# Performance work log

Measured on AMD Instinct MI355X. Metric: run time of the kernel, lower is better.

The kernel has to match this reference:

```python
import jax, jax.numpy as jnp
import numpy as np

EPS = 1e-5

def _bn(x, g, b):
    # BatchNorm1d in training mode: biased batch variance, eps=1e-5
    mu = jnp.mean(x, axis=0)
    var = jnp.var(x, axis=0)
    return g * (x - mu) * jax.lax.rsqrt(var + EPS) + b

def _prelu(x, a):
    return jnp.where(x >= 0, x, a * x)

def setup_inputs() -> dict:
    key = jax.random.key(0)
    ks = jax.random.split(key, 32)
    B, MF, E = 4096, 128, 64
    f32 = jnp.float32

    def lin_w(k, o, i):
        bound = 1.0 / np.sqrt(i)
        return jax.random.uniform(k, (o, i), f32, -bound, bound)

    def lin_b(k, o, i):
        bound = 1.0 / np.sqrt(i)
        return jax.random.uniform(k, (o,), f32, -bound, bound)

    def exp_w(k, e, o, i):
        bound = 1.0 / np.sqrt(i)
        return jax.random.uniform(k, (e, o, i), f32, -bound, bound)

    def exp_b(k, e, o, i):
        bound = 1.0 / np.sqrt(i)
        return jax.random.uniform(k, (e, o), f32, -bound, bound)

    quarter = jnp.full((1,), 0.25, f32)  # PReLU default init
    return {
        'm0': jax.random.normal(ks[0], (B, MF), f32),
        'x0': jax.random.normal(ks[1], (B, 64), f32),
        'mW1': lin_w(ks[2], 256, 128), 'mb1': lin_b(ks[3], 256, 128),
        'mg1': jnp.ones((256,), f32), 'mbe1': jnp.zeros((256,), f32), 'ma1': quarter,
        'mW2': lin_w(ks[4], 128, 256), 'mb2': lin_b(ks[5], 128, 256),
        'mg2': jnp.ones((128,), f32), 'mbe2': jnp.zeros((128,), f32), 'ma2': quarter,
        'mW3': lin_w(ks[6], 64, 128), 'mb3': lin_b(ks[7], 64, 128),
        'mg3': jnp.ones((64,), f32), 'mbe3': jnp.zeros((64,), f32), 'ma3': quarter,
        'Wenc0': exp_w(ks[8], E, 256, 64), 'benc0': exp_b(ks[9], E, 256, 64),
        'Wenc1': exp_w(ks[10], E, 256, 256), 'benc1': exp_b(ks[11], E, 256, 256),
        'Wdec0': exp_w(ks[12], E, 256, 256), 'bdec0': exp_b(ks[13], E, 256, 256),
        'Wdec1': exp_w(ks[14], E, 64, 256), 'bdec1': exp_b(ks[15], E, 64, 256),
        'bng': jnp.ones((256,), f32), 'bnb': jnp.zeros((256,), f32), 'a': quarter,
    }

def reference(m0, x0, mW1, mb1, mg1, mbe1, ma1, mW2, mb2, mg2, mbe2, ma2,
              mW3, mb3, mg3, mbe3, ma3, Wenc0, benc0, Wenc1, benc1,
              Wdec0, bdec0, Wdec1, bdec1, bng, bnb, a):
    # m_encoder (MNet): Linear+BN+PReLU x3 -> per-sample expert weights [B, 64]
    h = _prelu(_bn(m0 @ mW1.T + mb1, mg1, mbe1), ma1)
    h = _prelu(_bn(h @ mW2.T + mb2, mg2, mbe2), ma2)
    w = _prelu(_bn(h @ mW3.T + mb3, mg3, mbe3), ma3)  # [B, E]

    w_sum = jnp.sum(w)           # scalar sum over all B*E, as in torch code
    wn = w / w_sum               # [B, E]

    def experts(z, W, b):
        # all-experts dense combine: sum_e wn[b,e] * (z @ W_e^T + b_e)
        h = jnp.einsum('bi,eoi->beo', z, W) + b  # [B, E, O]
        return jnp.einsum('beo,be->bo', h, wn)

    # encoder: depth=2, BN+PReLU after each layer (shared bn(256) and PReLU)
    z = _prelu(_bn(experts(x0, Wenc0, benc0), bng, bnb), a)
    z = _prelu(_bn(experts(z, Wenc1, benc1), bng, bnb), a)
    # decoder: BN+PReLU on all but last layer
    y = _prelu(_bn(experts(z, Wdec0, bdec0), bng, bnb), a)
    y = experts(y, Wdec1, bdec1)  # [B, 64]
    return y
```

## Files before the change

kernel.cpp:

```cpp
#include <hip/hip_runtime.h>
#include <stdint.h>

#define BATCH 4096
#define NEXP 64

typedef __bf16 bf16x8 __attribute__((ext_vector_type(8)));
typedef float f32x4 __attribute__((ext_vector_type(4)));
typedef float f32x8 __attribute__((ext_vector_type(8)));
typedef unsigned int u32x4 __attribute__((ext_vector_type(4)));
typedef unsigned short u16x4 __attribute__((ext_vector_type(4)));
typedef unsigned short u16x8 __attribute__((ext_vector_type(8)));

__device__ __forceinline__ unsigned short f2bf(float f) {
  unsigned u = __builtin_bit_cast(unsigned, f);
  u += 0x7fffu + ((u >> 16) & 1u);
  return (unsigned short)(u >> 16);
}
__device__ __forceinline__ float bf2f(unsigned short h) {
  unsigned u = ((unsigned)h) << 16;
  return __builtin_bit_cast(float, u);
}

__device__ __forceinline__ void async_copy16(const void* g, void* l) {
  __builtin_amdgcn_global_load_lds(
      (const __attribute__((address_space(1))) void*)(uintptr_t)g,
      (__attribute__((address_space(3))) void*)(uintptr_t)l, 16, 0, 0);
}

enum { AM_PLAIN = 0, AM_BN = 1 };

template <int BM_, int BN_, int WR, int WC, int AMODE>
__global__ __launch_bounds__(256, 4) void gemm_k(
    const float* __restrict__ Af32, const float* __restrict__ scv,
    const float* __restrict__ shv, const float* __restrict__ alphaPtr,
    const unsigned short* __restrict__ PB, int K, int nsubsTot,
    float* __restrict__ Cp, const float* __restrict__ biasv, int N,
    int ktilesTot) {
  constexpr int MS = BM_ / 16;
  constexpr int NS = BN_ / 16;
  constexpr int WTM = BM_ / WR, WTN = BN_ / WC;
  constexpr int TM = WTM / 16, TN = WTN / 16;
  constexpr int PCH = MS / 2;

  __shared__ __align__(16) unsigned short As[2 * MS * 512];
  __shared__ __align__(16) unsigned short Bs[2 * NS * 512];

  const int tid = threadIdx.x;
  const int lane = tid & 63;
  const int wid = tid >> 6;
  const int wrow = wid / WC, wcol = wid % WC;

  const int m0 = blockIdx.x * BM_;
  const int ntile = blockIdx.y;
  const int n0 = ntile * BN_;

  float alpha = 0.f;
  if constexpr (AMODE == AM_BN) alpha = alphaPtr[0];

  f32x4 acc[TM][TN] = {};

  for (int kt = 0; kt < ktilesTot; ++kt) {
    const int k0 = kt * 64;

    for (int f = wid; f < 2 * NS; f += 4) {
      const int fkt = f / NS, fns = f % NS;
      const long fragIdx = (long)(k0 / 32 + fkt) * nsubsTot + (ntile * NS + fns);
      async_copy16(PB + fragIdx * 512 + lane * 8, &Bs[f * 512 + lane * 8]);
    }

#pragma unroll
    for (int p = 0; p < PCH; ++p) {
      const int id = p * 256 + tid;
      const int fA = id >> 6;
      const int q = id & 63;
      const int ksh = fA / MS, msub = fA % MS;
      const int kq = q >> 4, mrow = q & 15;
      const int m = msub * 16 + mrow;
      const int kg = k0 + ksh * 32 + kq * 8;
      const long mg = m0 + m;
      f32x8 vf;
      if constexpr (AMODE == AM_PLAIN) {
        const f32x4* src = (const f32x4*)(Af32 + mg * K + kg);
        f32x4 a0 = src[0], a1 = src[1];
#pragma unroll
        for (int j = 0; j < 4; ++j) { vf[j] = a0[j]; vf[4 + j] = a1[j]; }
      } else {
        const f32x4* src = (const f32x4*)(Af32 + mg * K + kg);
        f32x4 a0 = src[0], a1 = src[1];
        f32x4 s0 = *(const f32x4*)(scv + kg), s1 = *(const f32x4*)(scv + kg + 4);
        f32x4 h0 = *(const f32x4*)(shv + kg), h1 = *(const f32x4*)(shv + kg + 4);
#pragma unroll
        for (int j = 0; j < 4; ++j) {
          float v = fmaf(a0[j], s0[j], h0[j]);
          vf[j] = v >= 0.f ? v : alpha * v;
          float v2 = fmaf(a1[j], s1[j], h1[j]);
          vf[4 + j] = v2 >= 0.f ? v2 : alpha * v2;
        }
      }
      bf16x8 ob = __builtin_convertvector(vf, bf16x8);
      *(u16x8*)&As[id * 8] = __builtin_bit_cast(u16x8, ob);
    }
    __syncthreads();

#pragma unroll
    for (int ks = 0; ks < 2; ++ks) {
      bf16x8 af[TM], bfr[TN];
#pragma unroll
      for (int i = 0; i < TM; ++i) {
        const int msub = wrow * TM + i;
        af[i] = __builtin_bit_cast(
            bf16x8, *(const u32x4*)&As[(ks * MS + msub) * 512 + lane * 8]);
      }
#pragma unroll
      for (int j = 0; j < TN; ++j) {
        const int nsub = wcol * TN + j;
        bfr[j] = __builtin_bit_cast(
            bf16x8, *(const u32x4*)&Bs[(ks * NS + nsub) * 512 + lane * 8]);
      }
#pragma unroll
      for (int i = 0; i < TM; ++i)
#pragma unroll
        for (int j = 0; j < TN; ++j)
          acc[i][j] = __builtin_amdgcn_mfma_f32_16x16x32_bf16(af[i], bfr[j],
                                                              acc[i][j], 0, 0, 0);
    }
    __syncthreads();
  }

  const int q = lane >> 4, nn = lane & 15;
#pragma unroll
  for (int i = 0; i < TM; ++i) {
    const int rowb = m0 + wrow * WTM + i * 16 + q * 4;
#pragma unroll
    for (int j = 0; j < TN; ++j) {
      const int col = n0 + wcol * WTN + j * 16 + nn;
      const float bv = biasv ? biasv[col] : 0.f;
#pragma unroll
      for (int r = 0; r < 4; ++r)
        Cp[(long)(rowb + r) * N + col] = acc[i][j][r] + bv;
    }
  }
}

template <int BN_, int KE_, int EPB, int NTILE>
__global__ __launch_bounds__(256, 2) void egemm_k(
    const unsigned short* __restrict__ zpk, const float* __restrict__ wnT,
    const float* __restrict__ bias, const unsigned short* __restrict__ PB,
    float* __restrict__ Cbase, long partStride, int N, int nsubsTot) {
  constexpr int KT2 = KE_ / 32;
  constexpr int NS = BN_ / 16;
  constexpr int TN = NS / 4;
  constexpr int TM = 4;
  constexpr int NC = NTILE * (NEXP / EPB);
  constexpr int T = EPB * KT2;
  constexpr int U = ((KT2 & 3) == 0) ? 1 : (4 / KT2);

  const int tid = threadIdx.x, lane = tid & 63, wid = tid >> 6;
  const int bx = blockIdx.x;
  const int combo = bx % NC;
  const int mb = bx / NC;
  const int ntile = combo % NTILE;
  const int slice = combo / NTILE;
  const int e0 = slice * EPB;
  const int n0 = ntile * BN_;
  float* __restrict__ Cp = Cbase + (long)slice * partStride;
  const int nn = lane & 15, q = lane >> 4;

  const unsigned short* Aw = zpk + (long)mb * (KT2 * 4 * 512);
  u32x4 areg[TM][KT2];
#pragma unroll
  for (int i = 0; i < TM; ++i)
#pragma unroll
    for (int kt = 0; kt < KT2; ++kt)
      areg[i][kt] = *(const u32x4*)(Aw + (kt * 4 + i) * 512 + lane * 8);

  const long kstr = (long)nsubsTot * 512;
  const unsigned short* Bt = PB + (long)e0 * KT2 * kstr +
                             ((long)ntile * NS + wid * TN) * 512 + lane * 8;

  u32x4 ring[4][TN];
#pragma unroll
  for (int t = 0; t < 4; ++t)
#pragma unroll
    for (int j = 0; j < TN; ++j)
      ring[t][j] = *(const u32x4*)(Bt + (long)t * kstr + j * 512);

  f32x4 mainAcc[TM][TN] = {};

  for (int eb = 0; eb < EPB; eb += U) {
#pragma unroll
    for (int u = 0; u < U; ++u) {
      const int ei = eb + u;
      const int e = e0 + ei;
      f32x4 tmp[TM][TN];
#pragma unroll
      for (int j = 0; j < TN; ++j) {
        const float bv = bias[(long)e * N + n0 + wid * (TN * 16) + j * 16 + nn];
        f32x4 t4 = {bv, bv, bv, bv};
#pragma unroll
        for (int i = 0; i < TM; ++i) tmp[i][j] = t4;
      }
#pragma unroll
      for (int kt = 0; kt < KT2; ++kt) {
        const int slot = (u * KT2 + kt) & 3;
#pragma unroll
        for (int i = 0; i < TM; ++i) {
          bf16x8 af = __builtin_bit_cast(bf16x8, areg[i][kt]);
#pragma unroll
          for (int j = 0; j < TN; ++j)
            tmp[i][j] = __builtin_amdgcn_mfma_f32_16x16x32_bf16(
                af, __builtin_bit_cast(bf16x8, ring[slot][j]), tmp[i][j], 0, 0,
                0);
        }
        {
          const int t = ei * KT2 + kt;
          const int tl = (t + 4 < T) ? (t + 4) : (T - 1);
#pragma unroll
          for (int j = 0; j < TN; ++j)
            ring[slot][j] = *(const u32x4*)(Bt + (long)tl * kstr + j * 512);
        }
      }
#pragma unroll
      for (int i = 0; i < TM; ++i) {
        const int rowb = mb * 64 + i * 16 + q * 4;
        f32x4 wn4 = *(const f32x4*)(wnT + (long)e * BATCH + rowb);
#pragma unroll
        for (int j = 0; j < TN; ++j) mainAcc[i][j] += wn4 * tmp[i][j];
      }
    }
  }

#pragma unroll
  for (int i = 0; i < TM; ++i) {
    const int rowb = mb * 64 + i * 16 + q * 4;
#pragma unroll
    for (int j = 0; j < TN; ++j) {
      const int col = n0 + wid * (TN * 16) + j * 16 + nn;
#pragma unroll
      for (int r = 0; r < 4; ++r)
        Cp[(long)(rowb + r) * N + col] = mainAcc[i][j][r];
    }
  }
}

__global__ void hbuild_k(float* __restrict__ P, long partStride, int nparts,
                         int total4) {
  const int idx = blockIdx.x * 256 + threadIdx.x;
  if (idx >= total4) return;
  f32x4 s = *(const f32x4*)(P + (long)idx * 4);
  for (int p = 1; p < nparts; ++p)
    s += *(const f32x4*)(P + p * partStride + (long)idx * 4);
  *(f32x4*)(P + (long)idx * 4) = s;
}

__global__ void stats_k(const float* __restrict__ H, int C,
                        const float* __restrict__ g, const float* __restrict__ b,
                        float* __restrict__ scv, float* __restrict__ shv) {
  const int c0 = blockIdx.x * 4;
  f32x4 s = {0.f, 0.f, 0.f, 0.f}, s2 = {0.f, 0.f, 0.f, 0.f};
  for (int r = threadIdx.x; r < BATCH; r += 256) {
    f32x4 x = *(const f32x4*)(H + (long)r * C + c0);
    s += x;
    s2 += x * x;
  }
  __shared__ f32x4 sb[256], qb[256];
  sb[threadIdx.x] = s;
  qb[threadIdx.x] = s2;
  __syncthreads();
  for (int st = 128; st > 0; st >>= 1) {
    if (threadIdx.x < st) {
      sb[threadIdx.x] += sb[threadIdx.x + st];
      qb[threadIdx.x] += qb[threadIdx.x + st];
    }
    __syncthreads();
  }
  if (threadIdx.x < 4) {
    const int c = c0 + threadIdx.x;
    float mu = sb[0][threadIdx.x] * (1.f / BATCH);
    float var = qb[0][threadIdx.x] * (1.f / BATCH) - mu * mu;
    float isig = 1.f / sqrtf(var + 1e-5f);
    float sc_ = g[c] * isig;
    scv[c] = sc_;
    shv[c] = b[c] - mu * sc_;
  }
}

__global__ void zbuild_pk(const float* __restrict__ H,
                          const float* __restrict__ scv,
                          const float* __restrict__ shv,
                          const float* __restrict__ alphaPtr,
                          unsigned short* __restrict__ zpk) {
  const int c = blockIdx.x * 256 + threadIdx.x;
  const float alpha = alphaPtr[0];
  const int mb = c >> 11, r = c & 2047;
  const int kt = r >> 8, q2 = r & 255;
  const int msub = q2 >> 6, ln = q2 & 63;
  const int row = mb * 64 + msub * 16 + (ln & 15);
  const int col = kt * 32 + (ln >> 4) * 8;
  const float* src = H + (long)row * 256 + col;
  f32x4 a0 = *(const f32x4*)src, a1 = *(const f32x4*)(src + 4);
  f32x4 s0 = *(const f32x4*)(scv + col), s1 = *(const f32x4*)(scv + col + 4);
  f32x4 h0 = *(const f32x4*)(shv + col), h1 = *(const f32x4*)(shv + col + 4);
  u16x8 o;
#pragma unroll
  for (int j = 0; j < 4; ++j) {
    float v = fmaf(a0[j], s0[j], h0[j]);
    v = v >= 0.f ? v : alpha * v;
    o[j] = f2bf(v);
    float v2 = fmaf(a1[j], s1[j], h1[j]);
    v2 = v2 >= 0.f ? v2 : alpha * v2;
    o[4 + j] = f2bf(v2);
  }
  *(u16x8*)(zpk + (long)c * 8) = o;
}

__global__ void cast_pk(const float* __restrict__ x,
                        unsigned short* __restrict__ zpk) {
  const int c = blockIdx.x * 256 + threadIdx.x;
  const int mb = c >> 9, r = c & 511;
  const int kt = r >> 8, q2 = r & 255;
  const int msub = q2 >> 6, ln = q2 & 63;
  const int row = mb * 64 + msub * 16 + (ln & 15);
  const int col = kt * 32 + (ln >> 4) * 8;
  const float* src = x + (long)row * 64 + col;
  f32x4 a0 = *(const f32x4*)src, a1 = *(const f32x4*)(src + 4);
  u16x8 o;
#pragma unroll
  for (int j = 0; j < 4; ++j) {
    o[j] = f2bf(a0[j]);
    o[4 + j] = f2bf(a1[j]);
  }
  *(u16x8*)(zpk + (long)c * 8) = o;
}

__global__ void wbuild_k(const float* __restrict__ G, const float* __restrict__ scv,
                         const float* __restrict__ shv,
                         const float* __restrict__ alphaPtr,
                         float* __restrict__ w, float* __restrict__ wsum) {
  const int idx = blockIdx.x * 256 + threadIdx.x;
  const float alpha = alphaPtr[0];
  const int c0 = (idx * 4) & 63;
  f32x4 x = *(const f32x4*)(G + (long)idx * 4);
  f32x4 sv = *(const f32x4*)(scv + c0);
  f32x4 hv = *(const f32x4*)(shv + c0);
  f32x4 o;
  float part = 0.f;
#pragma unroll
  for (int j = 0; j < 4; ++j) {
    float v = fmaf(x[j], sv[j], hv[j]);
    v = v >= 0.f ? v : alpha * v;
    o[j] = v;
    part += v;
  }
  *(f32x4*)(w + (long)idx * 4) = o;
  __shared__ float sb[256];
  sb[threadIdx.x] = part;
  __syncthreads();
  for (int st = 128; st > 0; st >>= 1) {
    if (threadIdx.x < st) sb[threadIdx.x] += sb[threadIdx.x + st];
    __syncthreads();
  }
  if (threadIdx.x == 0) atomicAdd(wsum, sb[0]);
}

__global__ void inv_k(const float* __restrict__ wsum, float* __restrict__ invp) {
  if (threadIdx.x == 0 && blockIdx.x == 0) invp[0] = 1.0f / wsum[0];
}

__global__ void wntbuild_k(const float* __restrict__ w,
                           const float* __restrict__ invp,
                           float* __restrict__ wnT) {
  const int idx = blockIdx.x * 256 + threadIdx.x;
  const int e = idx >> 12, b = idx & 4095;
  wnT[idx] = w[(long)b * NEXP + e] * invp[0];
}

__global__ void prepack_k(const float* __restrict__ W, const float* __restrict__ bias,
                          unsigned short* __restrict__ PB, int O, int shI, int EI,
                          long totalChunks) {
  const long t = (long)blockIdx.x * 256 + threadIdx.x;
  if (t >= totalChunks) return;
  const int lane = (int)(t & 63);
  const long frag = t >> 6;
  const int nsubs = O / 16;
  const int nsub = (int)(frag % nsubs);
  const long ktile = frag / nsubs;
  const int n = nsub * 16 + (lane & 15);
  const int k = (int)(ktile * 32 + (lane >> 4) * 8);
  u16x8 o;
  if (k < EI) {
    const int e = k >> shI;
    const int i0 = k & ((1 << shI) - 1);
    const float* src = W + ((long)e * O + n) * (1 << shI) + i0;
    f32x4 a0 = *(const f32x4*)src;
    f32x4 a1 = *(const f32x4*)(src + 4);
#pragma unroll
    for (int j = 0; j < 4; ++j) {
      o[j] = f2bf(a0[j]);
      o[4 + j] = f2bf(a1[j]);
    }
  } else {
#pragma unroll
    for (int j = 0; j < 8; ++j) {
      const int ee = k + j - EI;
      o[j] = f2bf(bias[(long)ee * O + n]);
    }
  }
  *(u16x8*)(PB + t * 8) = o;
}

__global__ void reduceN_k(const float* __restrict__ P, long partStride, int nparts,
                          float* __restrict__ out, int total4) {
  const int idx = blockIdx.x * 256 + threadIdx.x;
  if (idx >= total4) return;
  f32x4 s = {0.f, 0.f, 0.f, 0.f};
  for (int p = 0; p < nparts; ++p) s += *(const f32x4*)(P + p * partStride + (long)idx * 4);
  *(f32x4*)(out + (long)idx * 4) = s;
}

extern "C" void kernel_launch(void* const* d_in, const int* in_sizes, int n_in,
                              void* d_out, int out_size, void* d_ws, size_t ws_size,
                              hipStream_t stream) {
  const float* m0 = (const float*)d_in[0];
  const float* x0 = (const float*)d_in[1];
  const float* mW1 = (const float*)d_in[2];
  const float* mb1 = (const float*)d_in[3];
  const float* mg1 = (const float*)d_in[4];
  const float* mbe1 = (const float*)d_in[5];
  const float* ma1 = (const float*)d_in[6];
  const float* mW2 = (const float*)d_in[7];
  const float* mb2 = (const float*)d_in[8];
  const float* mg2 = (const float*)d_in[9];
  const float* mbe2 = (const float*)d_in[10];
  const float* ma2 = (const float*)d_in[11];
  const float* mW3 = (const float*)d_in[12];
  const float* mb3 = (const float*)d_in[13];
  const float* mg3 = (const float*)d_in[14];
  const float* mbe3 = (const float*)d_in[15];
  const float* ma3 = (const float*)d_in[16];
  const float* Wenc0 = (const float*)d_in[17];
  const float* benc0 = (const float*)d_in[18];
  const float* Wenc1 = (const float*)d_in[19];
  const float* benc1 = (const float*)d_in[20];
  const float* Wdec0 = (const float*)d_in[21];
  const float* bdec0 = (const float*)d_in[22];
  const float* Wdec1 = (const float*)d_in[23];
  const float* bdec1 = (const float*)d_in[24];
  const float* bng = (const float*)d_in[25];
  const float* bnb = (const float*)d_in[26];
  const float* aexp = (const float*)d_in[27];

  const int SPL = 8, SPLD = 16;

  char* base = (char*)d_ws;
  size_t off = 0;
  auto alloc = [&](size_t bytes) {
    void* p = base + off;
    off = (off + bytes + 255) & ~(size_t)255;
    return p;
  };
  unsigned short* PB = (unsigned short*)alloc(16448L * 256 * 2);
  float* Pb = (float*)alloc((size_t)SPL * BATCH * 256 * 4);
  float* P0 = Pb;
  float* P1 = Pb + (long)BATCH * 256;
  unsigned short* zApk = (unsigned short*)alloc(BATCH * 256 * 2);
  unsigned short* zBpk = (unsigned short*)alloc(BATCH * 256 * 2);
  unsigned short* x0pk = (unsigned short*)alloc(BATCH * 64 * 2);
  float* wbuf = (float*)alloc(BATCH * 64 * 4);
  float* wnT = (float*)alloc((size_t)NEXP * BATCH * 4);
  float* scv = (float*)alloc(256 * 4);
  float* shv = (float*)alloc(256 * 4);
  float* wsum = (float*)alloc(256);
  float* invp = (float*)alloc(256);

  const dim3 blk(256);
  const long PS = BATCH * 256;

  prepack_k<<<16, blk, 0, stream>>>(mW1, nullptr, PB, 256, 7, 128, 4096);
  gemm_k<64, 128, 2, 2, AM_PLAIN><<<dim3(64, 2, 1), blk, 0, stream>>>(
      m0, nullptr, nullptr, nullptr, PB, 128, 16, P0, mb1, 256, 2);
  stats_k<<<64, blk, 0, stream>>>(P0, 256, mg1, mbe1, scv, shv);

  prepack_k<<<16, blk, 0, stream>>>(mW2, nullptr, PB, 128, 8, 256, 4096);
  gemm_k<64, 128, 2, 2, AM_BN><<<dim3(64, 1, 1), blk, 0, stream>>>(
      P0, scv, shv, ma1, PB, 256, 8, P1, mb2, 128, 4);
  stats_k<<<32, blk, 0, stream>>>(P1, 128, mg2, mbe2, scv, shv);

  prepack_k<<<4, blk, 0, stream>>>(mW3, nullptr, PB, 64, 7, 128, 1024);
  gemm_k<64, 64, 2, 2, AM_BN><<<dim3(64, 1, 1), blk, 0, stream>>>(
      P1, scv, shv, ma2, PB, 128, 4, P0, mb3, 64, 2);
  stats_k<<<16, blk, 0, stream>>>(P0, 64, mg3, mbe3, scv, shv);

  hipMemsetAsync(wsum, 0, 4, stream);
  wbuild_k<<<256, blk, 0, stream>>>(P0, scv, shv, ma3, wbuf, wsum);
  inv_k<<<1, 64, 0, stream>>>(wsum, invp);
  wntbuild_k<<<1024, blk, 0, stream>>>(wbuf, invp, wnT);
  cast_pk<<<128, blk, 0, stream>>>(x0, x0pk);

  prepack_k<<<512, blk, 0, stream>>>(Wenc0, nullptr, PB, 256, 6, 4096, 131072);
  egemm_k<128, 64, 8, 2><<<dim3(1024), blk, 0, stream>>>(
      x0pk, wnT, benc0, PB, Pb, PS, 256, 16);
  hbuild_k<<<1024, blk, 0, stream>>>(Pb, PS, SPL, 262144);
  stats_k<<<64, blk, 0, stream>>>(Pb, 256, bng, bnb, scv, shv);
  zbuild_pk<<<512, blk, 0, stream>>>(Pb, scv, shv, aexp, zApk);

  prepack_k<<<2048, blk, 0, stream>>>(Wenc1, nullptr, PB, 256, 8, 16384, 524288);
  egemm_k<128, 256, 8, 2><<<dim3(1024), blk, 0, stream>>>(
      zApk, wnT, benc1, PB, Pb, PS, 256, 16);
  hbuild_k<<<1024, blk, 0, stream>>>(Pb, PS, SPL, 262144);
  stats_k<<<64, blk, 0, stream>>>(Pb, 256, bng, bnb, scv, shv);
  zbuild_pk<<<512, blk, 0, stream>>>(Pb, scv, shv, aexp, zBpk);

  prepack_k<<<2048, blk, 0, stream>>>(Wdec0, nullptr, PB, 256, 8, 16384, 524288);
  egemm_k<128, 256, 8, 2><<<dim3(1024), blk, 0, stream>>>(
      zBpk, wnT, bdec0, PB, Pb, PS, 256, 16);
  hbuild_k<<<1024, blk, 0, stream>>>(Pb, PS, SPL, 262144);
  stats_k<<<64, blk, 0, stream>>>(Pb, 256, bng, bnb, scv, shv);
  zbuild_pk<<<512, blk, 0, stream>>>(Pb, scv, shv, aexp, zApk);

  prepack_k<<<512, blk, 0, stream>>>(Wdec1, nullptr, PB, 64, 8, 16384, 131072);
  egemm_k<64, 256, 4, 1><<<dim3(1024), blk, 0, stream>>>(
      zApk, wnT, bdec1, PB, Pb, (long)BATCH * 64, 64, 4);
  reduceN_k<<<256, blk, 0, stream>>>(Pb, (long)BATCH * 64, SPLD, (float*)d_out,
                                     65536);

  (void)in_sizes; (void)n_in; (void)out_size; (void)ws_size;
}
```

Before: 410.5 us.

## Batch weight prepacking, fuse partial reduction with BN stats, halve expert splits

```diff
diff --git a/kernel.cpp b/kernel.cpp
--- a/kernel.cpp
+++ b/kernel.cpp
@@ -15,10 +15,6 @@
   unsigned u = __builtin_bit_cast(unsigned, f);
   u += 0x7fffu + ((u >> 16) & 1u);
   return (unsigned short)(u >> 16);
-}
-__device__ __forceinline__ float bf2f(unsigned short h) {
-  unsigned u = ((unsigned)h) << 16;
-  return __builtin_bit_cast(float, u);
 }
 
 __device__ __forceinline__ void async_copy16(const void* g, void* l) {
@@ -166,6 +162,14 @@
   float* __restrict__ Cp = Cbase + (long)slice * partStride;
   const int nn = lane & 15, q = lane >> 4;
 
+  float bvAll[EPB * TN];
+#pragma unroll
+  for (int ei = 0; ei < EPB; ++ei)
+#pragma unroll
+    for (int j = 0; j < TN; ++j)
+      bvAll[ei * TN + j] =
+          bias[(long)(e0 + ei) * N + n0 + wid * (TN * 16) + j * 16 + nn];
+
   const unsigned short* Aw = zpk + (long)mb * (KT2 * 4 * 512);
   u32x4 areg[TM][KT2];
 #pragma unroll
@@ -195,7 +199,7 @@
       f32x4 tmp[TM][TN];
 #pragma unroll
       for (int j = 0; j < TN; ++j) {
-        const float bv = bias[(long)e * N + n0 + wid * (TN * 16) + j * 16 + nn];
+        const float bv = bvAll[ei * TN + j];
         f32x4 t4 = {bv, bv, bv, bv};
 #pragma unroll
         for (int i = 0; i < TM; ++i) tmp[i][j] = t4;
@@ -243,14 +247,34 @@
   }
 }
 
-__global__ void hbuild_k(float* __restrict__ P, long partStride, int nparts,
-                         int total4) {
-  const int idx = blockIdx.x * 256 + threadIdx.x;
-  if (idx >= total4) return;
-  f32x4 s = *(const f32x4*)(P + (long)idx * 4);
-  for (int p = 1; p < nparts; ++p)
-    s += *(const f32x4*)(P + p * partStride + (long)idx * 4);
-  *(f32x4*)(P + (long)idx * 4) = s;
+__global__ void hstats_k(float* __restrict__ P, long partStride, int nparts,
+                         int C, float* __restrict__ S1, float* __restrict__ S2) {
+  const int c0 = blockIdx.x * 4;
+  const int r0 = blockIdx.y * (BATCH / 8);
+  f32x4 s = {0.f, 0.f, 0.f, 0.f}, s2 = {0.f, 0.f, 0.f, 0.f};
+  for (int r = r0 + threadIdx.x; r < r0 + BATCH / 8; r += 256) {
+    f32x4 x = *(const f32x4*)(P + (long)r * C + c0);
+    for (int p = 1; p < nparts; ++p)
+      x += *(const f32x4*)(P + p * partStride + (long)r * C + c0);
+    *(f32x4*)(P + (long)r * C + c0) = x;
+    s += x;
+    s2 += x * x;
+  }
+  __shared__ f32x4 sb[256], qb[256];
+  sb[threadIdx.x] = s;
+  qb[threadIdx.x] = s2;
+  __syncthreads();
+  for (int st = 128; st > 0; st >>= 1) {
+    if (threadIdx.x < st) {
+      sb[threadIdx.x] += sb[threadIdx.x + st];
+      qb[threadIdx.x] += qb[threadIdx.x + st];
+    }
+    __syncthreads();
+  }
+  if (threadIdx.x < 4) {
+    atomicAdd(&S1[c0 + threadIdx.x], sb[0][threadIdx.x]);
+    atomicAdd(&S2[c0 + threadIdx.x], qb[0][threadIdx.x]);
+  }
 }
 
 __global__ void stats_k(const float* __restrict__ H, int C,
@@ -286,8 +310,10 @@
 }
 
 __global__ void zbuild_pk(const float* __restrict__ H,
-                          const float* __restrict__ scv,
-                          const float* __restrict__ shv,
+                          const float* __restrict__ S1,
+                          const float* __restrict__ S2,
+                          const float* __restrict__ g,
+                          const float* __restrict__ b,
                           const float* __restrict__ alphaPtr,
                           unsigned short* __restrict__ zpk) {
   const int c = blockIdx.x * 256 + threadIdx.x;
@@ -298,37 +324,24 @@
   const int row = mb * 64 + msub * 16 + (ln & 15);
   const int col = kt * 32 + (ln >> 4) * 8;
   const float* src = H + (long)row * 256 + col;
-  f32x4 a0 = *(const f32x4*)src, a1 = *(const f32x4*)(src + 4);
-  f32x4 s0 = *(const f32x4*)(scv + col), s1 = *(const f32x4*)(scv + col + 4);
-  f32x4 h0 = *(const f32x4*)(shv + col), h1 = *(const f32x4*)(shv + col + 4);
   u16x8 o;
 #pragma unroll
-  for (int j = 0; j < 4; ++j) {
-    float v = fmaf(a0[j], s0[j], h0[j]);
-    v = v >= 0.f ? v : alpha * v;
-    o[j] = f2bf(v);
-    float v2 = fmaf(a1[j], s1[j], h1[j]);
-    v2 = v2 >= 0.f ? v2 : alpha * v2;
-    o[4 + j] = f2bf(v2);
-  }
-  *(u16x8*)(zpk + (long)c * 8) = o;
-}
-
-__global__ void cast_pk(const float* __restrict__ x,
-                        unsigned short* __restrict__ zpk) {
-  const int c = blockIdx.x * 256 + threadIdx.x;
-  const int mb = c >> 9, r = c & 511;
-  const int kt = r >> 8, q2 = r & 255;
-  const int msub = q2 >> 6, ln = q2 & 63;
-  const int row = mb * 64 + msub * 16 + (ln & 15);
-  const int col = kt * 32 + (ln >> 4) * 8;
-  const float* src = x + (long)row * 64 + col;
-  f32x4 a0 = *(const f32x4*)src, a1 = *(const f32x4*)(src + 4);
-  u16x8 o;
-#pragma unroll
-  for (int j = 0; j < 4; ++j) {
-    o[j] = f2bf(a0[j]);
-    o[4 + j] = f2bf(a1[j]);
+  for (int h = 0; h < 2; ++h) {
+    f32x4 a = *(const f32x4*)(src + h * 4);
+    f32x4 s1 = *(const f32x4*)(S1 + col + h * 4);
+    f32x4 s2 = *(const f32x4*)(S2 + col + h * 4);
+    f32x4 gv = *(const f32x4*)(g + col + h * 4);
+    f32x4 bv = *(const f32x4*)(b + col + h * 4);
+#pragma unroll
+    for (int j = 0; j < 4; ++j) {
+      float mu = s1[j] * (1.f / BATCH);
+      float var = s2[j] * (1.f / BATCH) - mu * mu;
+      float sc_ = gv[j] / sqrtf(var + 1e-5f);
+      float sh_ = bv[j] - mu * sc_;
+      float v = fmaf(a[j], sc_, sh_);
+      v = v >= 0.f ? v : alpha * v;
+      o[h * 4 + j] = f2bf(v);
+    }
   }
   *(u16x8*)(zpk + (long)c * 8) = o;
 }
@@ -363,50 +376,69 @@
   if (threadIdx.x == 0) atomicAdd(wsum, sb[0]);
 }
 
-__global__ void inv_k(const float* __restrict__ wsum, float* __restrict__ invp) {
-  if (threadIdx.x == 0 && blockIdx.x == 0) invp[0] = 1.0f / wsum[0];
-}
-
-__global__ void wntbuild_k(const float* __restrict__ w,
-                           const float* __restrict__ invp,
-                           float* __restrict__ wnT) {
-  const int idx = blockIdx.x * 256 + threadIdx.x;
-  const int e = idx >> 12, b = idx & 4095;
-  wnT[idx] = w[(long)b * NEXP + e] * invp[0];
-}
-
-__global__ void prepack_k(const float* __restrict__ W, const float* __restrict__ bias,
-                          unsigned short* __restrict__ PB, int O, int shI, int EI,
-                          long totalChunks) {
-  const long t = (long)blockIdx.x * 256 + threadIdx.x;
-  if (t >= totalChunks) return;
-  const int lane = (int)(t & 63);
-  const long frag = t >> 6;
-  const int nsubs = O / 16;
+__global__ void wnTcast_k(const float* __restrict__ w,
+                          const float* __restrict__ wsum,
+                          float* __restrict__ wnT, const float* __restrict__ x0,
+                          unsigned short* __restrict__ x0pk) {
+  const int bx = blockIdx.x;
+  if (bx < 1024) {
+    const int idx = bx * 256 + threadIdx.x;
+    const int e = idx >> 12, b = idx & 4095;
+    wnT[idx] = w[(long)b * NEXP + e] * (1.0f / wsum[0]);
+  } else {
+    const int c = (bx - 1024) * 256 + threadIdx.x;
+    const int mb = c >> 9, r = c & 511;
+    const int kt = r >> 8, q2 = r & 255;
+    const int msub = q2 >> 6, ln = q2 & 63;
+    const int row = mb * 64 + msub * 16 + (ln & 15);
+    const int col = kt * 32 + (ln >> 4) * 8;
+    const float* src = x0 + (long)row * 64 + col;
+    f32x4 a0 = *(const f32x4*)src, a1 = *(const f32x4*)(src + 4);
+    u16x8 o;
+#pragma unroll
+    for (int j = 0; j < 4; ++j) {
+      o[j] = f2bf(a0[j]);
+      o[4 + j] = f2bf(a1[j]);
+    }
+    *(u16x8*)(x0pk + (long)c * 8) = o;
+  }
+}
+
+__global__ void prepackall_k(
+    const float* __restrict__ w0, const float* __restrict__ w1,
+    const float* __restrict__ w2, const float* __restrict__ w3,
+    const float* __restrict__ w4, const float* __restrict__ w5,
+    const float* __restrict__ w6, unsigned short* __restrict__ PB) {
+  const int t = blockIdx.x * 256 + threadIdx.x;
+  const float* W;
+  int nsubs, shI;
+  long loc;
+  if (t < 4096) { W = w0; nsubs = 16; shI = 7; loc = t; }
+  else if (t < 8192) { W = w1; nsubs = 8; shI = 8; loc = t - 4096; }
+  else if (t < 9216) { W = w2; nsubs = 4; shI = 7; loc = t - 8192; }
+  else if (t < 140288) { W = w3; nsubs = 16; shI = 6; loc = t - 9216; }
+  else if (t < 664576) { W = w4; nsubs = 16; shI = 8; loc = t - 140288; }
+  else if (t < 1188864) { W = w5; nsubs = 16; shI = 8; loc = t - 664576; }
+  else if (t < 1319936) { W = w6; nsubs = 4; shI = 8; loc = t - 1188864; }
+  else return;
+  const int lane = (int)(loc & 63);
+  const long frag = loc >> 6;
   const int nsub = (int)(frag % nsubs);
   const long ktile = frag / nsubs;
   const int n = nsub * 16 + (lane & 15);
   const int k = (int)(ktile * 32 + (lane >> 4) * 8);
+  const int e = k >> shI;
+  const int i0 = k & ((1 << shI) - 1);
+  const int O = nsubs * 16;
+  const float* src = W + ((long)e * O + n) * (1 << shI) + i0;
+  f32x4 a0 = *(const f32x4*)src, a1 = *(const f32x4*)(src + 4);
   u16x8 o;
-  if (k < EI) {
-    const int e = k >> shI;
-    const int i0 = k & ((1 << shI) - 1);
-    const float* src = W + ((long)e * O + n) * (1 << shI) + i0;
-    f32x4 a0 = *(const f32x4*)src;
-    f32x4 a1 = *(const f32x4*)(src + 4);
-#pragma unroll
-    for (int j = 0; j < 4; ++j) {
-      o[j] = f2bf(a0[j]);
-      o[4 + j] = f2bf(a1[j]);
-    }
-  } else {
-#pragma unroll
-    for (int j = 0; j < 8; ++j) {
-      const int ee = k + j - EI;
-      o[j] = f2bf(bias[(long)ee * O + n]);
-    }
-  }
-  *(u16x8*)(PB + t * 8) = o;
+#pragma unroll
+  for (int j = 0; j < 4; ++j) {
+    o[j] = f2bf(a0[j]);
+    o[4 + j] = f2bf(a1[j]);
+  }
+  *(u16x8*)(PB + (long)t * 8) = o;
 }
 
 __global__ void reduceN_k(const float* __restrict__ P, long partStride, int nparts,
@@ -414,7 +446,8 @@
   const int idx = blockIdx.x * 256 + threadIdx.x;
   if (idx >= total4) return;
   f32x4 s = {0.f, 0.f, 0.f, 0.f};
-  for (int p = 0; p < nparts; ++p) s += *(const f32x4*)(P + p * partStride + (long)idx * 4);
+  for (int p = 0; p < nparts; ++p)
+    s += *(const f32x4*)(P + p * partStride + (long)idx * 4);
   *(f32x4*)(out + (long)idx * 4) = s;
 }
 
@@ -450,7 +483,8 @@
   const float* bnb = (const float*)d_in[26];
   const float* aexp = (const float*)d_in[27];
 
-  const int SPL = 8, SPLD = 16;
+  const int SPL = 4;
+  const int SPLD = 8;
 
   char* base = (char*)d_ws;
   size_t off = 0;
@@ -459,7 +493,9 @@
     off = (off + bytes + 255) & ~(size_t)255;
     return p;
   };
-  unsigned short* PB = (unsigned short*)alloc(16448L * 256 * 2);
+  unsigned short* PB = (unsigned short*)alloc(1319936L * 16);
+  const long CO_mW2 = 4096, CO_mW3 = 8192, CO_e0 = 9216, CO_e1 = 140288,
+             CO_d0 = 664576, CO_d1 = 1188864;
   float* Pb = (float*)alloc((size_t)SPL * BATCH * 256 * 4);
   float* P0 = Pb;
   float* P1 = Pb + (long)BATCH * 256;
@@ -470,57 +506,48 @@
   float* wnT = (float*)alloc((size_t)NEXP * BATCH * 4);
   float* scv = (float*)alloc(256 * 4);
   float* shv = (float*)alloc(256 * 4);
-  float* wsum = (float*)alloc(256);
-  float* invp = (float*)alloc(256);
+  float* zeroBuf = (float*)alloc(8192);
+  float* wsum = zeroBuf;
+  float* S1a = zeroBuf + 256, *S2a = zeroBuf + 512;
+  float* S1b = zeroBuf + 768, *S2b = zeroBuf + 1024;
+  float* S1c = zeroBuf + 1280, *S2c = zeroBuf + 1536;
 
   const dim3 blk(256);
   const long PS = BATCH * 256;
 
-  prepack_k<<<16, blk, 0, stream>>>(mW1, nullptr, PB, 256, 7, 128, 4096);
+  hipMemsetAsync(zeroBuf, 0, 8192, stream);
+  prepackall_k<<<5156, blk, 0, stream>>>(mW1, mW2, mW3, Wenc0, Wenc1, Wdec0,
+                                         Wdec1, PB);
+
   gemm_k<64, 128, 2, 2, AM_PLAIN><<<dim3(64, 2, 1), blk, 0, stream>>>(
       m0, nullptr, nullptr, nullptr, PB, 128, 16, P0, mb1, 256, 2);
   stats_k<<<64, blk, 0, stream>>>(P0, 256, mg1, mbe1, scv, shv);
-
-  prepack_k<<<16, blk, 0, stream>>>(mW2, nullptr, PB, 128, 8, 256, 4096);
   gemm_k<64, 128, 2, 2, AM_BN><<<dim3(64, 1, 1), blk, 0, stream>>>(
-      P0, scv, shv, ma1, PB, 256, 8, P1, mb2, 128, 4);
+      P0, scv, shv, ma1, PB + CO_mW2 * 8, 256, 8, P1, mb2, 128, 4);
   stats_k<<<32, blk, 0, stream>>>(P1, 128, mg2, mbe2, scv, shv);
-
-  prepack_k<<<4, blk, 0, stream>>>(mW3, nullptr, PB, 64, 7, 128, 1024);
   gemm_k<64, 64, 2, 2, AM_BN><<<dim3(64, 1, 1), blk, 0, stream>>>(
-      P1, scv, shv, ma2, PB, 128, 4, P0, mb3, 64, 2);
+      P1, scv, shv, ma2, PB + CO_mW3 * 8, 128, 4, P0, mb3, 64, 2);
   stats_k<<<16, blk, 0, stream>>>(P0, 64, mg3, mbe3, scv, shv);
-
-  hipMemsetAsync(wsum, 0, 4, stream);
   wbuild_k<<<256, blk, 0, stream>>>(P0, scv, shv, ma3, wbuf, wsum);
-  inv_k<<<1, 64, 0, stream>>>(wsum, invp);
-  wntbuild_k<<<1024, blk, 0, stream>>>(wbuf, invp, wnT);
-  cast_pk<<<128, blk, 0, stream>>>(x0, x0pk);
-
-  prepack_k<<<512, blk, 0, stream>>>(Wenc0, nullptr, PB, 256, 6, 4096, 131072);
-  egemm_k<128, 64, 8, 2><<<dim3(1024), blk, 0, stream>>>(
-      x0pk, wnT, benc0, PB, Pb, PS, 256, 16);
-  hbuild_k<<<1024, blk, 0, stream>>>(Pb, PS, SPL, 262144);
-  stats_k<<<64, blk, 0, stream>>>(Pb, 256, bng, bnb, scv, shv);
-  zbuild_pk<<<512, blk, 0, stream>>>(Pb, scv, shv, aexp, zApk);
-
-  prepack_k<<<2048, blk, 0, stream>>>(Wenc1, nullptr, PB, 256, 8, 16384, 524288);
-  egemm_k<128, 256, 8, 2><<<dim3(1024), blk, 0, stream>>>(
-      zApk, wnT, benc1, PB, Pb, PS, 256, 16);
-  hbuild_k<<<1024, blk, 0, stream>>>(Pb, PS, SPL, 262144);
-  stats_k<<<64, blk, 0, stream>>>(Pb, 256, bng, bnb, scv, shv);
-  zbuild_pk<<<512, blk, 0, stream>>>(Pb, scv, shv, aexp, zBpk);
-
-  prepack_k<<<2048, blk, 0, stream>>>(Wdec0, nullptr, PB, 256, 8, 16384, 524288);
-  egemm_k<128, 256, 8, 2><<<dim3(1024), blk, 0, stream>>>(
-      zBpk, wnT, bdec0, PB, Pb, PS, 256, 16);
-  hbuild_k<<<1024, blk, 0, stream>>>(Pb, PS, SPL, 262144);
-  stats_k<<<64, blk, 0, stream>>>(Pb, 256, bng, bnb, scv, shv);
-  zbuild_pk<<<512, blk, 0, stream>>>(Pb, scv, shv, aexp, zApk);
-
-  prepack_k<<<512, blk, 0, stream>>>(Wdec1, nullptr, PB, 64, 8, 16384, 131072);
-  egemm_k<64, 256, 4, 1><<<dim3(1024), blk, 0, stream>>>(
-      zApk, wnT, bdec1, PB, Pb, (long)BATCH * 64, 64, 4);
+  wnTcast_k<<<1152, blk, 0, stream>>>(wbuf, wsum, wnT, x0, x0pk);
+
+  egemm_k<128, 64, 16, 2><<<dim3(512), blk, 0, stream>>>(
+      x0pk, wnT, benc0, PB + CO_e0 * 8, Pb, PS, 256, 16);
+  hstats_k<<<dim3(64, 8), blk, 0, stream>>>(Pb, PS, SPL, 256, S1a, S2a);
+  zbuild_pk<<<512, blk, 0, stream>>>(Pb, S1a, S2a, bng, bnb, aexp, zApk);
+
+  egemm_k<128, 256, 16, 2><<<dim3(512), blk, 0, stream>>>(
+      zApk, wnT, benc1, PB + CO_e1 * 8, Pb, PS, 256, 16);
+  hstats_k<<<dim3(64, 8), blk, 0, stream>>>(Pb, PS, SPL, 256, S1b, S2b);
+  zbuild_pk<<<512, blk, 0, stream>>>(Pb, S1b, S2b, bng, bnb, aexp, zBpk);
+
+  egemm_k<128, 256, 16, 2><<<dim3(512), blk, 0, stream>>>(
+      zBpk, wnT, bdec0, PB + CO_d0 * 8, Pb, PS, 256, 16);
+  hstats_k<<<dim3(64, 8), blk, 0, stream>>>(Pb, PS, SPL, 256, S1c, S2c);
+  zbuild_pk<<<512, blk, 0, stream>>>(Pb, S1c, S2c, bng, bnb, aexp, zApk);
+
+  egemm_k<64, 256, 8, 1><<<dim3(512), blk, 0, stream>>>(
+      zApk, wnT, bdec1, PB + CO_d1 * 8, Pb, (long)BATCH * 64, 64, 4);
   reduceN_k<<<256, blk, 0, stream>>>(Pb, (long)BATCH * 64, SPLD, (float*)d_out,
                                      65536);
 
```

New measurement: 410.8 us. No clear change (+0.1%).
